# Performance work log

Measured on AMD Instinct MI355X. Metric: run time of the kernel, lower is better.

The kernel has to match this reference:

```python
import jax, jax.numpy as jnp
import numpy as np

EPS = 1e-5


def hetero_layernorm(x, node_type, gamma, beta):
    # LayerNorm over feature dim with per-node-type affine params.
    mu = jnp.mean(x, axis=-1, keepdims=True)
    var = jnp.mean(jnp.square(x - mu), axis=-1, keepdims=True)
    xn = (x - mu) * jax.lax.rsqrt(var + EPS)
    return xn * gamma[node_type] + beta[node_type]


def rgcn_conv(y, edge_src, edge_dst, edge_type, W_rel, W_root):
    # Transform per relation first (R small), then gather per-edge message.
    n = y.shape[0]
    h = jnp.einsum('nd,rde->rne', y, W_rel)          # [R, N, d]
    msg = h[edge_type, edge_src]                     # [E, d] gather
    agg = jax.ops.segment_sum(msg, edge_dst, num_segments=n)  # [N, d]
    return agg + y @ W_root


def hetero_mlp(y, node_type, W_mlp, b_mlp):
    # Per-node-type linear: compute for all T types, then select.
    n = y.shape[0]
    h = jnp.einsum('nd,tde->tne', y, W_mlp) + b_mlp[:, None, :]  # [T, N, d]
    return h[node_type, jnp.arange(n)]


def setup_inputs() -> dict:
    key = jax.random.key(0)
    ks = jax.random.split(key, 8)
    N, E, D, T, R = 50000, 800000, 128, 4, 8
    x = jax.random.normal(ks[0], (N, D), dtype=jnp.float32)
    edge_src = jax.random.randint(ks[1], (E,), 0, N, dtype=jnp.int32)
    edge_dst = jax.random.randint(ks[2], (E,), 0, N, dtype=jnp.int32)
    node_type = jax.random.randint(ks[3], (N,), 0, T, dtype=jnp.int32)
    edge_type = jax.random.randint(ks[4], (E,), 0, R, dtype=jnp.int32)
    # Scale weights ~ 1/sqrt(fan_in) for stable magnitudes.
    s = 1.0 / np.sqrt(D)
    W_rel = jax.random.normal(ks[5], (R, D, D), dtype=jnp.float32) * s
    W_root = jax.random.normal(ks[6], (D, D), dtype=jnp.float32) * s
    W_mlp = jax.random.normal(ks[7], (T, D, D), dtype=jnp.float32) * s
    return {
        'x': x, 'edge_src': edge_src, 'edge_dst': edge_dst,
        'node_type': node_type, 'edge_type': edge_type,
        'conv_gamma': jnp.ones((T, D), jnp.float32),
        'conv_beta': jnp.zeros((T, D), jnp.float32),
        'W_rel': W_rel, 'W_root': W_root,
        'mlp_gamma': jnp.ones((T, D), jnp.float32),
        'mlp_beta': jnp.zeros((T, D), jnp.float32),
        'W_mlp': W_mlp, 'b_mlp': jnp.zeros((T, D), jnp.float32),
    }


def reference(x, edge_src, edge_dst, node_type, edge_type,
              conv_gamma, conv_beta, W_rel, W_root,
              mlp_gamma, mlp_beta, W_mlp, b_mlp):
    # Norm -> Act -> (Dropout p=0, eval) -> Conv -> Residual
    y = hetero_layernorm(x, node_type, conv_gamma, conv_beta)
    y = jax.nn.relu(y)
    x = x + rgcn_conv(y, edge_src, edge_dst, edge_type, W_rel, W_root)
    # Norm -> Act -> (Dropout p=0, eval) -> MLP -> Residual
    y = hetero_layernorm(x, node_type, mlp_gamma, mlp_beta)
    y = jax.nn.relu(y)
    x = x + hetero_mlp(y, node_type, W_mlp, b_mlp)
    return x
```

## Files before the change

### kernel.cpp

```cpp
#include <hip/hip_runtime.h>
#include <hip/hip_bf16.h>

#define D 128
#define EPS 1e-5f
#define CHK 8192
#define P2CAP 6144

typedef __attribute__((ext_vector_type(8))) short short8;
typedef __attribute__((ext_vector_type(4))) float float4v;

__device__ inline ushort f2bf(float f) {
    __hip_bfloat16 b = __float2bfloat16(f);
    return *reinterpret_cast<ushort*>(&b);
}
__device__ inline float bf_lo(uint u) { return __uint_as_float(u << 16); }
__device__ inline float bf_hi(uint u) { return __uint_as_float(u & 0xffff0000u); }

__global__ void k_ln1cvt(const float* __restrict__ x, const int* __restrict__ ntp,
                         const float* __restrict__ gamma, const float* __restrict__ beta,
                         ushort* __restrict__ y,
                         const float* __restrict__ Wrel, const float* __restrict__ Wroot,
                         const float* __restrict__ Wmlp, ushort* __restrict__ Wt, int N) {
    __shared__ ushort t[128][136];
    if (blockIdx.x < 13) {
        int m = blockIdx.x;
        const float* src = (m == 0) ? Wroot
                         : (m <= 8) ? Wrel + (size_t)(m - 1) * D * D
                                    : Wmlp + (size_t)(m - 9) * D * D;
        for (int i = threadIdx.x; i < D * D; i += 256) {
            int k = i >> 7, n = i & 127;
            t[n][k] = f2bf(src[i]);
        }
        __syncthreads();
        ushort* dst = Wt + (size_t)m * D * D;
        for (int i = threadIdx.x; i < D * D; i += 256) {
            int frag = i >> 9;
            int lane = (i >> 3) & 63;
            int j = i & 7;
            int nt = frag >> 2, ks = frag & 3;
            int n = nt * 16 + (lane & 15);
            int k = ks * 32 + (lane >> 4) * 8 + j;
            dst[i] = t[n][k];
        }
        return;
    }
    int n = (blockIdx.x - 13) * 4 + (threadIdx.x >> 6);
    if (n >= N) return;
    int l = threadIdx.x & 63;
    float2 v = *(const float2*)(x + (size_t)n * D + 2 * l);
    float s = v.x + v.y, s2 = v.x * v.x + v.y * v.y;
    #pragma unroll
    for (int o = 32; o; o >>= 1) { s += __shfl_xor(s, o, 64); s2 += __shfl_xor(s2, o, 64); }
    float mu = s * (1.0f / D);
    float var = s2 * (1.0f / D) - mu * mu;
    float inv = rsqrtf(var + EPS);
    int tt = ntp[n];
    float2 g = *(const float2*)(gamma + tt * D + 2 * l);
    float2 b = *(const float2*)(beta + tt * D + 2 * l);
    float a0 = fmaxf((v.x - mu) * inv * g.x + b.x, 0.0f);
    float a1 = fmaxf((v.y - mu) * inv * g.y + b.y, 0.0f);
    ((uint*)(y + (size_t)n * D))[l] = ((uint)f2bf(a1) << 16) | f2bf(a0);
}

__global__ void k_c1(const int* __restrict__ edst, int* __restrict__ hist, int E, int B) {
    __shared__ int cnt[256];
    int c = blockIdx.x, tid = threadIdx.x;
    cnt[tid] = 0;
    __syncthreads();
    #pragma unroll 4
    for (int k = 0; k < CHK / 256; ++k) {
        int e = c * CHK + k * 256 + tid;
        if (e < E) atomicAdd(&cnt[edst[e] >> 8], 1);
    }
    __syncthreads();
    if (tid < B) hist[c * B + tid] = cnt[tid];
}
__global__ void k_c2(const int* __restrict__ hist, int* __restrict__ chunkoff,
                     int* __restrict__ bucktot, int C, int B) {
    __shared__ int v[128];
    int b = blockIdx.x, t = threadIdx.x;
    v[t] = (t < C) ? hist[t * B + b] : 0;
    __syncthreads();
    if (t == 0) {
        int s = 0;
        for (int c = 0; c < C; ++c) { int x = v[c]; v[c] = s; s += x; }
        bucktot[b] = s;
    }
    __syncthreads();
    if (t < C) chunkoff[t * B + b] = v[t];
}
__global__ void k_p1s(const int* __restrict__ edst, const int* __restrict__ esrc,
                      const int* __restrict__ etyp, const int* __restrict__ bucktot,
                      const int* __restrict__ chunkoff, uint* __restrict__ edata,
                      int E, int B) {
    __shared__ int ps[256];
    __shared__ int base[256];
    __shared__ int cnt[256];
    int c = blockIdx.x, tid = threadIdx.x;
    int bt = (tid < B) ? bucktot[tid] : 0;
    ps[tid] = bt;
    __syncthreads();
    for (int o = 1; o < 256; o <<= 1) {
        int v = (tid >= o) ? ps[tid - o] : 0;
        __syncthreads();
        ps[tid] += v;
        __syncthreads();
    }
    base[tid] = (ps[tid] - bt) + ((tid < B) ? chunkoff[c * B + tid] : 0);
    cnt[tid] = 0;
    __syncthreads();
    #pragma unroll 4
    for (int k = 0; k < CHK / 256; ++k) {
        int e = c * CHK + k * 256 + tid;
        if (e < E) {
            int d = edst[e];
            int b = d >> 8;
            int r = atomicAdd(&cnt[b], 1);
            edata[base[b] + r] =
                ((uint)esrc[e] << 12) | ((uint)(d & 255) << 4) | (uint)etyp[e];
        }
    }
}
__global__ void k_p2(const uint* __restrict__ edata, const int* __restrict__ bucktot,
                     uint* __restrict__ epack, int* __restrict__ offs,
                     int N, int E, int B) {
    __shared__ int ps[256];
    __shared__ uint ed[P2CAP];
    __shared__ int cnt[256], off[256], cur[256];
    int b = blockIdx.x, tid = threadIdx.x;
    int bt = (tid < B) ? bucktot[tid] : 0;
    ps[tid] = bt;
    __syncthreads();
    for (int o = 1; o < 256; o <<= 1) {
        int v = (tid >= o) ? ps[tid - o] : 0;
        __syncthreads();
        ps[tid] += v;
        __syncthreads();
    }
    int j0 = ps[b] - ((b < B) ? bucktot[b] : 0);
    int count = ps[b] - j0;
    if (count > P2CAP) count = P2CAP;
    for (int i = tid; i < count; i += 256) ed[i] = edata[j0 + i];
    cnt[tid] = 0;
    __syncthreads();
    for (int i = tid; i < count; i += 256) atomicAdd(&cnt[(ed[i] >> 4) & 255], 1);
    __syncthreads();
    if (tid == 0) {
        int s = 0;
        for (int i = 0; i < 256; ++i) { off[i] = s; cur[i] = s; s += cnt[i]; }
    }
    __syncthreads();
    for (int i = tid; i < count; i += 256) {
        uint v = ed[i];
        int dl = (v >> 4) & 255;
        int r = atomicAdd(&cur[dl], 1);
        epack[j0 + r] = ((v & 15u) << 28) | (v >> 12);
    }
    int v = b * 256 + tid;
    if (v < N) offs[v] = j0 + off[tid];
    if (b == 0 && tid == 0) offs[N] = E;
}

__global__ void k_zagg(const ushort* __restrict__ ybuf, const int* __restrict__ offs,
                       const uint* __restrict__ epack, ushort* __restrict__ zbuf, int N) {
    int wave = threadIdx.x >> 6;
    int l = threadIdx.x & 63;
    int v = blockIdx.x * 4 + wave;
    if (v >= N) return;
    float2 a0 = {0.f,0.f}, a1 = {0.f,0.f}, a2 = {0.f,0.f}, a3 = {0.f,0.f};
    float2 a4 = {0.f,0.f}, a5 = {0.f,0.f}, a6 = {0.f,0.f}, a7 = {0.f,0.f};
    const uint* yb = (const uint*)ybuf;
    int j = offs[v], e1 = offs[v + 1];

#define ZACC(P, U) do {                                                   \
        float lo = bf_lo(U), hi = bf_hi(U);                               \
        switch ((P) >> 28) {                                              \
            case 0: a0.x += lo; a0.y += hi; break;                        \
            case 1: a1.x += lo; a1.y += hi; break;                        \
            case 2: a2.x += lo; a2.y += hi; break;                        \
            case 3: a3.x += lo; a3.y += hi; break;                        \
            case 4: a4.x += lo; a4.y += hi; break;                        \
            case 5: a5.x += lo; a5.y += hi; break;                        \
            case 6: a6.x += lo; a6.y += hi; break;                        \
            default: a7.x += lo; a7.y += hi; break;                       \
        }                                                                 \
    } while (0)

    while (j < e1) {
        int chunk = min(64, e1 - j);
        uint pl = (j + l < e1) ? epack[j + l] : 0;
        int i = 0;
        for (; i + 3 < chunk; i += 4) {
            uint p0 = __shfl(pl, i, 64);
            uint p1 = __shfl(pl, i + 1, 64);
            uint p2 = __shfl(pl, i + 2, 64);
            uint p3 = __shfl(pl, i + 3, 64);
            uint u0 = yb[(size_t)(p0 & 0x0FFFFFFFu) * 64 + l];
            uint u1 = yb[(size_t)(p1 & 0x0FFFFFFFu) * 64 + l];
            uint u2 = yb[(size_t)(p2 & 0x0FFFFFFFu) * 64 + l];
            uint u3 = yb[(size_t)(p3 & 0x0FFFFFFFu) * 64 + l];
            ZACC(p0, u0); ZACC(p1, u1); ZACC(p2, u2); ZACC(p3, u3);
        }
        for (; i < chunk; ++i) {
            uint p = __shfl(pl, i, 64);
            uint u = yb[(size_t)(p & 0x0FFFFFFFu) * 64 + l];
            ZACC(p, u);
        }
        j += chunk;
    }
#undef ZACC
    uint* zrow = (uint*)(zbuf + (size_t)v * 1024);
    zrow[0 * 64 + l] = ((uint)f2bf(a0.y) << 16) | f2bf(a0.x);
    zrow[1 * 64 + l] = ((uint)f2bf(a1.y) << 16) | f2bf(a1.x);
    zrow[2 * 64 + l] = ((uint)f2bf(a2.y) << 16) | f2bf(a2.x);
    zrow[3 * 64 + l] = ((uint)f2bf(a3.y) << 16) | f2bf(a3.x);
    zrow[4 * 64 + l] = ((uint)f2bf(a4.y) << 16) | f2bf(a4.x);
    zrow[5 * 64 + l] = ((uint)f2bf(a5.y) << 16) | f2bf(a5.x);
    zrow[6 * 64 + l] = ((uint)f2bf(a6.y) << 16) | f2bf(a6.x);
    zrow[7 * 64 + l] = ((uint)f2bf(a7.y) << 16) | f2bf(a7.x);
}

__device__ __forceinline__ void aload4(short8 (&d)[2][4], const ushort* p0,
                                       const ushort* p1, int off, int ao) {
    #pragma unroll
    for (int ks = 0; ks < 4; ++ks) {
        d[0][ks] = *(const short8*)(p0 + off + ks * 32 + ao);
        d[1][ks] = *(const short8*)(p1 + off + ks * 32 + ao);
    }
}
__device__ __forceinline__ void mm2x8(float4v (&acc)[2][8], const short8 (&a)[2][4],
                                      const ushort* __restrict__ wp, int lane) {
    #pragma unroll
    for (int nt = 0; nt < 8; ++nt) {
        #pragma unroll
        for (int ks = 0; ks < 4; ++ks) {
            short8 b = *(const short8*)(wp + (((nt * 4 + ks) * 64 + lane) << 3));
            acc[0][nt] = __builtin_amdgcn_mfma_f32_16x16x32_bf16(a[0][ks], b, acc[0][nt], 0, 0, 0);
            acc[1][nt] = __builtin_amdgcn_mfma_f32_16x16x32_bf16(a[1][ks], b, acc[1][nt], 0, 0, 0);
        }
    }
}

__launch_bounds__(128, 2)
__global__ void k_gm(const ushort* __restrict__ ybuf, const ushort* __restrict__ zbuf,
                     const ushort* __restrict__ Wt, const float* __restrict__ x,
                     const int* __restrict__ ntp,
                     const float* __restrict__ gamma, const float* __restrict__ beta,
                     const float* __restrict__ bmlp, float* __restrict__ out, int N) {
    __shared__ ushort ysm[2][32][136];
    int tid = threadIdx.x;
    int wave = tid >> 6, lane = tid & 63;
    int quad = lane >> 4, l15 = lane & 15;
    int ao = quad * 8;
    int base = blockIdx.x * 64 + wave * 32;

    const ushort* yrow0 = ybuf + (size_t)min(base + l15,      N - 1) * 128;
    const ushort* yrow1 = ybuf + (size_t)min(base + 16 + l15, N - 1) * 128;
    const ushort* zrow0 = zbuf + (size_t)min(base + l15,      N - 1) * 1024;
    const ushort* zrow1 = zbuf + (size_t)min(base + 16 + l15, N - 1) * 1024;

    float4v acc[2][8];
    #pragma unroll
    for (int g = 0; g < 2; ++g)
        #pragma unroll
        for (int nt = 0; nt < 8; ++nt) acc[g][nt] = (float4v){0.f, 0.f, 0.f, 0.f};

    short8 aC[2][4], aN[2][4];
    aload4(aC, yrow0, yrow1, 0, ao);
    aload4(aN, zrow0, zrow1, 0, ao);
    mm2x8(acc, aC, Wt, lane);
    #pragma unroll
    for (int mm = 0; mm < 4; ++mm) {
        aload4(aC, zrow0, zrow1, (2 * mm + 1) * 128, ao);
        mm2x8(acc, aN, Wt + (size_t)(2 * mm + 1) * 16384, lane);
        if (mm < 3) aload4(aN, zrow0, zrow1, (2 * mm + 2) * 128, ao);
        mm2x8(acc, aC, Wt + (size_t)(2 * mm + 2) * 16384, lane);
    }

    int ty[2][4];
    #pragma unroll
    for (int g = 0; g < 2; ++g) {
        int gb = base + g * 16;
        float s[4] = {0.f, 0.f, 0.f, 0.f}, s2[4] = {0.f, 0.f, 0.f, 0.f};
        #pragma unroll
        for (int nt = 0; nt < 8; ++nt) {
            int col = nt * 16 + l15;
            #pragma unroll
            for (int r = 0; r < 4; ++r) {
                int row = gb + quad * 4 + r;
                float xv = (row < N) ? x[(size_t)row * D + col] : 0.f;
                float t = acc[g][nt][r] + xv;
                acc[g][nt][r] = t;
                s[r] += t; s2[r] += t * t;
            }
        }
        #pragma unroll
        for (int r = 0; r < 4; ++r) {
            #pragma unroll
            for (int o = 1; o < 16; o <<= 1) {
                s[r]  += __shfl_xor(s[r],  o, 64);
                s2[r] += __shfl_xor(s2[r], o, 64);
            }
        }
        #pragma unroll
        for (int r = 0; r < 4; ++r) {
            int rc = min(gb + quad * 4 + r, N - 1);
            ty[g][r] = ntp[rc];
            float mu  = s[r] * (1.0f / D);
            float var = s2[r] * (1.0f / D) - mu * mu;
            float inv = rsqrtf(var + EPS);
            int lrow = g * 16 + quad * 4 + r;
            #pragma unroll
            for (int nt = 0; nt < 8; ++nt) {
                int col = nt * 16 + l15;
                float yn = fmaxf((acc[g][nt][r] - mu) * inv * gamma[ty[g][r] * D + col]
                                 + beta[ty[g][r] * D + col], 0.f);
                ysm[wave][lrow][col] = f2bf(yn);
            }
        }
    }
    short8 a2[2][4];
    #pragma unroll
    for (int g = 0; g < 2; ++g) {
        const ushort* myrow = &ysm[wave][g * 16 + l15][0];
        #pragma unroll
        for (int ks = 0; ks < 4; ++ks) a2[g][ks] = *(const short8*)(myrow + ks * 32 + ao);
    }

    const ushort* W0 = Wt + (size_t)9  * D * D;
    const ushort* W1 = Wt + (size_t)10 * D * D;
    const ushort* W2 = Wt + (size_t)11 * D * D;
    const ushort* W3 = Wt + (size_t)12 * D * D;
    #pragma unroll
    for (int nt = 0; nt < 8; ++nt) {
        float4v c[2][4];
        #pragma unroll
        for (int g = 0; g < 2; ++g)
            #pragma unroll
            for (int t = 0; t < 4; ++t) c[g][t] = (float4v){0.f, 0.f, 0.f, 0.f};
        #pragma unroll
        for (int ks = 0; ks < 4; ++ks) {
            int fo = ((nt * 4 + ks) * 64 + lane) << 3;
            short8 b0 = *(const short8*)(W0 + fo);
            short8 b1 = *(const short8*)(W1 + fo);
            short8 b2 = *(const short8*)(W2 + fo);
            short8 b3 = *(const short8*)(W3 + fo);
            #pragma unroll
            for (int g = 0; g < 2; ++g) {
                c[g][0] = __builtin_amdgcn_mfma_f32_16x16x32_bf16(a2[g][ks], b0, c[g][0], 0, 0, 0);
                c[g][1] = __builtin_amdgcn_mfma_f32_16x16x32_bf16(a2[g][ks], b1, c[g][1], 0, 0, 0);
                c[g][2] = __builtin_amdgcn_mfma_f32_16x16x32_bf16(a2[g][ks], b2, c[g][2], 0, 0, 0);
                c[g][3] = __builtin_amdgcn_mfma_f32_16x16x32_bf16(a2[g][ks], b3, c[g][3], 0, 0, 0);
            }
        }
        int col = nt * 16 + l15;
        #pragma unroll
        for (int g = 0; g < 2; ++g) {
            #pragma unroll
            for (int r = 0; r < 4; ++r) {
                int row = base + g * 16 + quad * 4 + r;
                if (row < N) {
                    int t = ty[g][r];
                    float v = (t == 0) ? c[g][0][r] : (t == 1) ? c[g][1][r]
                            : (t == 2) ? c[g][2][r] : c[g][3][r];
                    out[(size_t)row * D + col] = acc[g][nt][r] + v + bmlp[t * D + col];
                }
            }
        }
    }
}

extern "C" void kernel_launch(void* const* d_in, const int* in_sizes, int n_in,
                              void* d_out, int out_size, void* d_ws, size_t ws_size,
                              hipStream_t stream) {
    const float* x          = (const float*)d_in[0];
    const int*   esrc       = (const int*)d_in[1];
    const int*   edst       = (const int*)d_in[2];
    const int*   ntyp       = (const int*)d_in[3];
    const int*   etyp       = (const int*)d_in[4];
    const float* conv_gamma = (const float*)d_in[5];
    const float* conv_beta  = (const float*)d_in[6];
    const float* W_rel      = (const float*)d_in[7];
    const float* W_root     = (const float*)d_in[8];
    const float* mlp_gamma  = (const float*)d_in[9];
    const float* mlp_beta   = (const float*)d_in[10];
    const float* W_mlp      = (const float*)d_in[11];
    const float* b_mlp      = (const float*)d_in[12];
    float* out = (float*)d_out;

    int N = in_sizes[0] / D;
    int E = in_sizes[1];
    int C = (E + CHK - 1) / CHK;
    int B = (N + 255) / 256;

    char* p = (char*)d_ws;
    auto take = [&p](size_t bytes) { char* q = p; p += (bytes + 255) & ~(size_t)255; return q; };
    ushort* ybuf    = (ushort*)take((size_t)N * D * 2);
    ushort* zbuf    = (ushort*)take((size_t)N * 1024 * 2);
    ushort* Wt      = (ushort*)take((size_t)13 * D * D * 2);
    uint*   edata   = (uint*)take((size_t)E * 4);
    uint*   epack   = (uint*)take((size_t)E * 4);
    int*    offs    = (int*)take((size_t)(N + 1) * 4);
    int*    hist    = (int*)take((size_t)C * B * 4);
    int*    chunkoff= (int*)take((size_t)C * B * 4);
    int*    bucktot = (int*)take((size_t)B * 4);

    k_ln1cvt<<<13 + (N + 3) / 4, 256, 0, stream>>>(x, ntyp, conv_gamma, conv_beta,
                                                   ybuf, W_rel, W_root, W_mlp, Wt, N);

    k_c1<<<C, 256, 0, stream>>>(edst, hist, E, B);
    k_c2<<<B, 128, 0, stream>>>(hist, chunkoff, bucktot, C, B);
    k_p1s<<<C, 256, 0, stream>>>(edst, esrc, etyp, bucktot, chunkoff, edata, E, B);
    k_p2<<<B, 256, 0, stream>>>(edata, bucktot, epack, offs, N, E, B);

    k_zagg<<<(N + 3) / 4, 256, 0, stream>>>(ybuf, offs, epack, zbuf, N);

    k_gm<<<(N + 63) / 64, 128, 0, stream>>>(ybuf, zbuf, Wt, x, ntyp,
                                            mlp_gamma, mlp_beta, b_mlp, out, N);
}
```

Baseline: 297.4 us.

## Stage weight tiles into LDS via async global-to-LDS loads in fused GEMM kernel

The final fused GEMM kernel now copies each half-matrix of bf16 weights into a double-buffered shared-memory tile with global_load_lds, and all waves read B fragments from LDS instead of each wave fetching them from global memory. The block grows from 2 to 4 waves (128 rows per block) so each staged weight tile is reused by more rows. The MLP stage processes one node-type weight matrix at a time, selecting per-row results into an accumulator. This cuts redundant global and L2 weight traffic, at the cost of extra barriers, more LDS per block, and more live registers.

```diff
diff --git a/kernel.cpp b/kernel.cpp
--- a/kernel.cpp
+++ b/kernel.cpp
@@ -8,6 +8,9 @@
 
 typedef __attribute__((ext_vector_type(8))) short short8;
 typedef __attribute__((ext_vector_type(4))) float float4v;
+
+#define AS1 __attribute__((address_space(1)))
+#define AS3 __attribute__((address_space(3)))
 
 __device__ inline ushort f2bf(float f) {
     __hip_bfloat16 b = __float2bfloat16(f);
@@ -220,6 +223,19 @@
     zrow[7 * 64 + l] = ((uint)f2bf(a7.y) << 16) | f2bf(a7.x);
 }
 
+__device__ __forceinline__ void gl_lds16(const void* g, void* l) {
+    __builtin_amdgcn_global_load_lds((const AS1 void*)g, (AS3 void*)l, 16, 0, 0);
+}
+__device__ __forceinline__ void stage_half(const ushort* __restrict__ Wt, int q,
+                                           ushort* bsm0, int wave, int lane) {
+    const char* g = (const char*)Wt + (size_t)q * 16384 + lane * 16;
+    char* l = (char*)bsm0 + (q & 1) * 16384;
+    #pragma unroll
+    for (int i = 0; i < 4; ++i) {
+        int c = i * 4 + wave;
+        gl_lds16(g + c * 1024, l + c * 1024);
+    }
+}
 __device__ __forceinline__ void aload4(short8 (&d)[2][4], const ushort* p0,
                                        const ushort* p1, int off, int ao) {
     #pragma unroll
@@ -228,31 +244,47 @@
         d[1][ks] = *(const short8*)(p1 + off + ks * 32 + ao);
     }
 }
-__device__ __forceinline__ void mm2x8(float4v (&acc)[2][8], const short8 (&a)[2][4],
-                                      const ushort* __restrict__ wp, int lane) {
-    #pragma unroll
-    for (int nt = 0; nt < 8; ++nt) {
+__device__ __forceinline__ void convHalf(float4v (&acc)[2][8], const short8 (&a)[2][4],
+                                         const ushort* bsm_h, int h, int lane) {
+    #pragma unroll
+    for (int nt4 = 0; nt4 < 4; ++nt4) {
         #pragma unroll
         for (int ks = 0; ks < 4; ++ks) {
-            short8 b = *(const short8*)(wp + (((nt * 4 + ks) * 64 + lane) << 3));
-            acc[0][nt] = __builtin_amdgcn_mfma_f32_16x16x32_bf16(a[0][ks], b, acc[0][nt], 0, 0, 0);
-            acc[1][nt] = __builtin_amdgcn_mfma_f32_16x16x32_bf16(a[1][ks], b, acc[1][nt], 0, 0, 0);
-        }
-    }
-}
-
-__launch_bounds__(128, 2)
+            short8 b = *(const short8*)(bsm_h + (((nt4 * 4 + ks) * 64 + lane) << 3));
+            acc[0][h * 4 + nt4] = __builtin_amdgcn_mfma_f32_16x16x32_bf16(
+                a[0][ks], b, acc[0][h * 4 + nt4], 0, 0, 0);
+            acc[1][h * 4 + nt4] = __builtin_amdgcn_mfma_f32_16x16x32_bf16(
+                a[1][ks], b, acc[1][h * 4 + nt4], 0, 0, 0);
+        }
+    }
+}
+__device__ __forceinline__ void mlpHalf(float4v (&ct)[2][4], const short8 (&a2)[2][4],
+                                        const ushort* bsm_h, int lane) {
+    #pragma unroll
+    for (int nt4 = 0; nt4 < 4; ++nt4) {
+        #pragma unroll
+        for (int ks = 0; ks < 4; ++ks) {
+            short8 b = *(const short8*)(bsm_h + (((nt4 * 4 + ks) * 64 + lane) << 3));
+            ct[0][nt4] = __builtin_amdgcn_mfma_f32_16x16x32_bf16(a2[0][ks], b, ct[0][nt4], 0, 0, 0);
+            ct[1][nt4] = __builtin_amdgcn_mfma_f32_16x16x32_bf16(a2[1][ks], b, ct[1][nt4], 0, 0, 0);
+        }
+    }
+}
+
+__launch_bounds__(256, 2)
 __global__ void k_gm(const ushort* __restrict__ ybuf, const ushort* __restrict__ zbuf,
                      const ushort* __restrict__ Wt, const float* __restrict__ x,
                      const int* __restrict__ ntp,
                      const float* __restrict__ gamma, const float* __restrict__ beta,
                      const float* __restrict__ bmlp, float* __restrict__ out, int N) {
-    __shared__ ushort ysm[2][32][136];
+    __shared__ ushort bsm[2][8192];
+    __shared__ ushort ysm[4][32][140];
+    ushort* bsm0 = &bsm[0][0];
     int tid = threadIdx.x;
     int wave = tid >> 6, lane = tid & 63;
     int quad = lane >> 4, l15 = lane & 15;
     int ao = quad * 8;
-    int base = blockIdx.x * 64 + wave * 32;
+    int base = blockIdx.x * 128 + wave * 32;
 
     const ushort* yrow0 = ybuf + (size_t)min(base + l15,      N - 1) * 128;
     const ushort* yrow1 = ybuf + (size_t)min(base + 16 + l15, N - 1) * 128;
@@ -266,15 +298,21 @@
         for (int nt = 0; nt < 8; ++nt) acc[g][nt] = (float4v){0.f, 0.f, 0.f, 0.f};
 
     short8 aC[2][4], aN[2][4];
+    stage_half(Wt, 0, bsm0, wave, lane);
     aload4(aC, yrow0, yrow1, 0, ao);
     aload4(aN, zrow0, zrow1, 0, ao);
-    mm2x8(acc, aC, Wt, lane);
-    #pragma unroll
-    for (int mm = 0; mm < 4; ++mm) {
-        aload4(aC, zrow0, zrow1, (2 * mm + 1) * 128, ao);
-        mm2x8(acc, aN, Wt + (size_t)(2 * mm + 1) * 16384, lane);
-        if (mm < 3) aload4(aN, zrow0, zrow1, (2 * mm + 2) * 128, ao);
-        mm2x8(acc, aC, Wt + (size_t)(2 * mm + 2) * 16384, lane);
+    __syncthreads();
+
+    #pragma unroll
+    for (int m = 0; m < 9; ++m) {
+        short8 (&cur)[2][4] = (m & 1) ? aN : aC;
+        stage_half(Wt, 2 * m + 1, bsm0, wave, lane);
+        convHalf(acc, cur, bsm0, 0, lane);
+        __syncthreads();
+        stage_half(Wt, 2 * m + 2, bsm0, wave, lane);
+        convHalf(acc, cur, bsm0 + 8192, 1, lane);
+        if (m < 7) aload4(cur, zrow0, zrow1, (m + 1) * 128, ao);
+        __syncthreads();
     }
 
     int ty[2][4];
@@ -327,32 +365,52 @@
         for (int ks = 0; ks < 4; ++ks) a2[g][ks] = *(const short8*)(myrow + ks * 32 + ao);
     }
 
-    const ushort* W0 = Wt + (size_t)9  * D * D;
-    const ushort* W1 = Wt + (size_t)10 * D * D;
-    const ushort* W2 = Wt + (size_t)11 * D * D;
-    const ushort* W3 = Wt + (size_t)12 * D * D;
+    float4v oSel[2][8];
+    #pragma unroll
+    for (int g = 0; g < 2; ++g)
+        #pragma unroll
+        for (int nt = 0; nt < 8; ++nt) oSel[g][nt] = (float4v){0.f, 0.f, 0.f, 0.f};
+
+    #pragma unroll
+    for (int tm = 0; tm < 4; ++tm) {
+        stage_half(Wt, 19 + 2 * tm, bsm0, wave, lane);
+        {
+            float4v ct[2][4];
+            #pragma unroll
+            for (int g = 0; g < 2; ++g)
+                #pragma unroll
+                for (int n4 = 0; n4 < 4; ++n4) ct[g][n4] = (float4v){0.f, 0.f, 0.f, 0.f};
+            mlpHalf(ct, a2, bsm0, lane);
+            #pragma unroll
+            for (int g = 0; g < 2; ++g)
+                #pragma unroll
+                for (int n4 = 0; n4 < 4; ++n4)
+                    #pragma unroll
+                    for (int r = 0; r < 4; ++r)
+                        if (ty[g][r] == tm) oSel[g][n4][r] = ct[g][n4][r];
+        }
+        __syncthreads();
+        if (tm < 3) stage_half(Wt, 20 + 2 * tm, bsm0, wave, lane);
+        {
+            float4v ct[2][4];
+            #pragma unroll
+            for (int g = 0; g < 2; ++g)
+                #pragma unroll
+                for (int n4 = 0; n4 < 4; ++n4) ct[g][n4] = (float4v){0.f, 0.f, 0.f, 0.f};
+            mlpHalf(ct, a2, bsm0 + 8192, lane);
+            #pragma unroll
+            for (int g = 0; g < 2; ++g)
+                #pragma unroll
+                for (int n4 = 0; n4 < 4; ++n4)
+                    #pragma unroll
+                    for (int r = 0; r < 4; ++r)
+                        if (ty[g][r] == tm) oSel[g][4 + n4][r] = ct[g][n4][r];
+        }
+        if (tm < 3) __syncthreads();
+    }
+
     #pragma unroll
     for (int nt = 0; nt < 8; ++nt) {
-        float4v c[2][4];
-        #pragma unroll
-        for (int g = 0; g < 2; ++g)
-            #pragma unroll
-            for (int t = 0; t < 4; ++t) c[g][t] = (float4v){0.f, 0.f, 0.f, 0.f};
-        #pragma unroll
-        for (int ks = 0; ks < 4; ++ks) {
-            int fo = ((nt * 4 + ks) * 64 + lane) << 3;
-            short8 b0 = *(const short8*)(W0 + fo);
-            short8 b1 = *(const short8*)(W1 + fo);
-            short8 b2 = *(const short8*)(W2 + fo);
-            short8 b3 = *(const short8*)(W3 + fo);
-            #pragma unroll
-            for (int g = 0; g < 2; ++g) {
-                c[g][0] = __builtin_amdgcn_mfma_f32_16x16x32_bf16(a2[g][ks], b0, c[g][0], 0, 0, 0);
-                c[g][1] = __builtin_amdgcn_mfma_f32_16x16x32_bf16(a2[g][ks], b1, c[g][1], 0, 0, 0);
-                c[g][2] = __builtin_amdgcn_mfma_f32_16x16x32_bf16(a2[g][ks], b2, c[g][2], 0, 0, 0);
-                c[g][3] = __builtin_amdgcn_mfma_f32_16x16x32_bf16(a2[g][ks], b3, c[g][3], 0, 0, 0);
-            }
-        }
         int col = nt * 16 + l15;
         #pragma unroll
         for (int g = 0; g < 2; ++g) {
@@ -361,9 +419,8 @@
                 int row = base + g * 16 + quad * 4 + r;
                 if (row < N) {
                     int t = ty[g][r];
-                    float v = (t == 0) ? c[g][0][r] : (t == 1) ? c[g][1][r]
-                            : (t == 2) ? c[g][2][r] : c[g][3][r];
-                    out[(size_t)row * D + col] = acc[g][nt][r] + v + bmlp[t * D + col];
+                    out[(size_t)row * D + col] =
+                        acc[g][nt][r] + oSel[g][nt][r] + bmlp[t * D + col];
                 }
             }
         }
@@ -415,6 +472,6 @@
 
     k_zagg<<<(N + 3) / 4, 256, 0, stream>>>(ybuf, offs, epack, zbuf, N);
 
-    k_gm<<<(N + 63) / 64, 128, 0, stream>>>(ybuf, zbuf, Wt, x, ntyp,
-                                            mlp_gamma, mlp_beta, b_mlp, out, N);
-}
+    k_gm<<<(N + 127) / 128, 256, 0, stream>>>(ybuf, zbuf, Wt, x, ntyp,
+                                              mlp_gamma, mlp_beta, b_mlp, out, N);
+}
```

After: 347.1 us. 1.17x slower.
